# Optimization experiments

Measured on AMD Instinct MI355X. Metric: run time of the kernel, lower is better.

The kernel has to match this reference:

```python
import jax, jax.numpy as jnp
import numpy as np

DIM = 1024
NUM_HEADS = 16
HEAD_DIM = DIM // NUM_HEADS

def setup_inputs() -> dict:
    key = jax.random.key(0)
    ks = jax.random.split(key, 5)
    s = 1.0 / np.sqrt(DIM)
    x = jax.random.normal(ks[0], (2, 2048, DIM), dtype=jnp.float32)
    W_qkv = jax.random.uniform(ks[1], (DIM, 3 * DIM), dtype=jnp.float32, minval=-s, maxval=s)
    b_qkv = jax.random.uniform(ks[2], (3 * DIM,), dtype=jnp.float32, minval=-s, maxval=s)
    W_out = jax.random.uniform(ks[3], (DIM, DIM), dtype=jnp.float32, minval=-s, maxval=s)
    b_out = jax.random.uniform(ks[4], (DIM,), dtype=jnp.float32, minval=-s, maxval=s)
    return {"x": x, "W_qkv": W_qkv, "b_qkv": b_qkv, "W_out": W_out, "b_out": b_out}

def reference(x, W_qkv, b_qkv, W_out, b_out):
    B, S, _ = x.shape
    qkv = x @ W_qkv + b_qkv                       # [B,S,3*dim]
    q, k, v = jnp.split(qkv, 3, axis=-1)
    # [B,S,dim] -> [B,H,S,hd]
    def to_heads(t):
        return t.reshape(B, S, NUM_HEADS, HEAD_DIM).transpose(0, 2, 1, 3)
    q, k, v = to_heads(q), to_heads(k), to_heads(v)
    scale = HEAD_DIM ** -0.5
    scores = jnp.einsum('bhqd,bhkd->bhqk', q, k) * scale
    attn = jax.nn.softmax(scores, axis=-1)
    out = jnp.einsum('bhqk,bhkd->bhqd', attn, v)  # [B,H,S,hd]
    out = out.transpose(0, 2, 1, 3).reshape(B, S, DIM)
    return out @ W_out + b_out
```

## Files before the change

### kernel.cpp

```cpp
#include <hip/hip_runtime.h>
#include <math.h>

#define DIMM    1024
#define NHEADS  16
#define HDIM    64
#define BATCH   2
#define SEQ     2048
#define ROWS    (BATCH*SEQ)

typedef _Float16 f16x8 __attribute__((ext_vector_type(8)));
typedef _Float16 f16x4 __attribute__((ext_vector_type(4)));
typedef float    f32x4 __attribute__((ext_vector_type(4)));

__device__ inline void gl_lds16(const void* g, void* l) {
    __builtin_amdgcn_global_load_lds(
        (const __attribute__((address_space(1))) void*)g,
        (__attribute__((address_space(3))) void*)l, 16, 0, 0);
}

__global__ __launch_bounds__(256)
void cvt_kernel(const float* __restrict__ in, _Float16* __restrict__ out, int n8)
{
    int i = blockIdx.x * 256 + threadIdx.x;
    if (i >= n8) return;
    const float4 a = *(const float4*)(in + (size_t)i * 8);
    const float4 b = *(const float4*)(in + (size_t)i * 8 + 4);
    f16x8 o;
    o[0] = (_Float16)a.x; o[1] = (_Float16)a.y; o[2] = (_Float16)a.z; o[3] = (_Float16)a.w;
    o[4] = (_Float16)b.x; o[5] = (_Float16)b.y; o[6] = (_Float16)b.z; o[7] = (_Float16)b.w;
    *(f16x8*)(out + (size_t)i * 8) = o;
}

__global__ __launch_bounds__(256)
void transpose_cvt_kernel(const float* __restrict__ in, _Float16* __restrict__ out,
                          int K, int N)
{
    __shared__ float tile[64][65];
    const int k0 = blockIdx.y * 64, n0 = blockIdx.x * 64;
    const int t = threadIdx.x;
    {
        const int c4 = (t & 15) * 4;
        const int r  = t >> 4;
        #pragma unroll
        for (int i = 0; i < 4; i++) {
            const int rr = r + 16 * i;
            float4 v = *(const float4*)(in + (size_t)(k0 + rr) * N + n0 + c4);
            tile[rr][c4] = v.x; tile[rr][c4 + 1] = v.y;
            tile[rr][c4 + 2] = v.z; tile[rr][c4 + 3] = v.w;
        }
    }
    __syncthreads();
    #pragma unroll
    for (int i = 0; i < 2; i++) {
        const int seg = t + 256 * i;
        const int n   = seg >> 3;
        const int kc  = (seg & 7) * 8;
        f16x8 o;
        #pragma unroll
        for (int j = 0; j < 8; j++) o[j] = (_Float16)tile[kc + j][n];
        *(f16x8*)(out + (size_t)(n0 + n) * K + k0 + kc) = o;
    }
}

__global__ __launch_bounds__(256)
void vtranspose_kernel(const _Float16* __restrict__ qkvh, _Float16* __restrict__ vt)
{
    __shared__ _Float16 tile[64][72];
    const int kt = blockIdx.x;
    const int bh = blockIdx.y;
    const int b  = bh >> 4, h = bh & 15;
    const int t  = threadIdx.x;
    {
        const int key = t >> 2, c4 = (t & 3) * 16;
        const _Float16* src = qkvh + ((size_t)(b * SEQ + kt * 64 + key)) * (3 * DIMM)
                              + 2 * DIMM + h * HDIM + c4;
        f16x8 v0 = *(const f16x8*)src;
        f16x8 v1 = *(const f16x8*)(src + 8);
        #pragma unroll
        for (int j = 0; j < 8; j++) {
            tile[c4 + j][key]     = v0[j];
            tile[c4 + 8 + j][key] = v1[j];
        }
    }
    __syncthreads();
    {
        const int d = t >> 2, k4 = (t & 3) * 16;
        f16x8 o0, o1;
        #pragma unroll
        for (int j = 0; j < 8; j++) { o0[j] = tile[d][k4 + j]; o1[j] = tile[d][k4 + 8 + j]; }
        _Float16* dst = vt + ((size_t)bh * 64 + d) * SEQ + kt * 64 + k4;
        *(f16x8*)dst       = o0;
        *(f16x8*)(dst + 8) = o1;
    }
}

template<int OUT_F16>
__global__ __launch_bounds__(256)
void hgemm_bias_kernel(const _Float16* __restrict__ A, const _Float16* __restrict__ Bt,
                       const float* __restrict__ bias, void* __restrict__ Cout,
                       int N, int K)
{
    __shared__ _Float16 As[128 * 32];
    __shared__ _Float16 Bs[128 * 32];

    const int t    = threadIdx.x;
    const int w    = t >> 6, lane = t & 63;
    const int quad = lane >> 4, l16 = lane & 15;
    const int wr   = w >> 1, wc = w & 1;
    const int row0 = blockIdx.y * 128, col0 = blockIdx.x * 128;

    f32x4 acc[4][4];
    #pragma unroll
    for (int i = 0; i < 4; i++)
        #pragma unroll
        for (int j = 0; j < 4; j++)
            #pragma unroll
            for (int r = 0; r < 4; r++) acc[i][j][r] = 0.f;

    const int p0 = w * 128 + lane;
    const int p1 = p0 + 64;
    const int rA0 = p0 >> 2, kq0 = (p0 & 3) ^ ((p0 >> 4) & 3);
    const int rA1 = p1 >> 2, kq1 = (p1 & 3) ^ ((p1 >> 4) & 3);

    const _Float16* gA0 = A  + (size_t)(row0 + rA0) * K + kq0 * 8;
    const _Float16* gA1 = A  + (size_t)(row0 + rA1) * K + kq1 * 8;
    const _Float16* gB0 = Bt + (size_t)(col0 + rA0) * K + kq0 * 8;
    const _Float16* gB1 = Bt + (size_t)(col0 + rA1) * K + kq1 * 8;
    _Float16* lA0 = As + p0 * 8;
    _Float16* lA1 = As + p1 * 8;
    _Float16* lB0 = Bs + p0 * 8;
    _Float16* lB1 = Bs + p1 * 8;

    const int sx    = quad ^ ((l16 >> 2) & 3);
    const int abase = ((wr * 64 + l16) * 4 + sx) * 8;
    const int bbase = ((wc * 64 + l16) * 4 + sx) * 8;

    const int niter = K >> 5;
    for (int it = 0; it < niter; it++) {
        __syncthreads();
        gl_lds16(gA0, lA0); gl_lds16(gA1, lA1);
        gl_lds16(gB0, lB0); gl_lds16(gB1, lB1);
        gA0 += 32; gA1 += 32; gB0 += 32; gB1 += 32;
        __syncthreads();

        f16x8 af[4], bf[4];
        #pragma unroll
        for (int i = 0; i < 4; i++) {
            af[i] = *(const f16x8*)(As + abase + i * 512);
            bf[i] = *(const f16x8*)(Bs + bbase + i * 512);
        }
        #pragma unroll
        for (int i = 0; i < 4; i++)
            #pragma unroll
            for (int j = 0; j < 4; j++)
                acc[i][j] = __builtin_amdgcn_mfma_f32_16x16x32_f16(af[i], bf[j], acc[i][j], 0, 0, 0);
    }

    #pragma unroll
    for (int j = 0; j < 4; j++) {
        const int col = col0 + wc * 64 + j * 16 + l16;
        const float bv = bias[col];
        #pragma unroll
        for (int i = 0; i < 4; i++) {
            const int row = row0 + wr * 64 + i * 16 + quad * 4;
            #pragma unroll
            for (int r = 0; r < 4; r++) {
                const float v = acc[i][j][r] + bv;
                if (OUT_F16)
                    ((_Float16*)Cout)[(size_t)(row + r) * N + col] = (_Float16)v;
                else
                    ((float*)Cout)[(size_t)(row + r) * N + col] = v;
            }
        }
    }
}

__global__ __launch_bounds__(256, 4)
void flash_attn_kernel(const _Float16* __restrict__ qkv,
                       const _Float16* __restrict__ vtg,
                       _Float16* __restrict__ out)
{
    const int qt = blockIdx.x;
    const int bh = blockIdx.y;
    const int b  = bh >> 4, h = bh & 15;
    const int t    = threadIdx.x;
    const int w    = t >> 6;
    const int lane = t & 63;
    const int quad = lane >> 4;
    const int l16  = lane & 15;
    const int sw   = l16 & 7;

    __shared__ __align__(16) _Float16 Qs [64 * 64];
    __shared__ __align__(16) _Float16 Ks [64 * 64];
    __shared__ __align__(16) _Float16 Vts[64 * 64];
    __shared__ __align__(16) _Float16 Ps [64 * 72];

    const int q0 = qt * 64;
    const size_t rstr = 3 * DIMM;
    const _Float16* qbase = qkv + (size_t)b * SEQ * rstr;

    #pragma unroll
    for (int i = 0; i < 2; i++) {
        const int seg = t + 256 * i;
        const int row = seg >> 3, bp = seg & 7;
        const int lb  = bp ^ (row & 7);
        gl_lds16(qbase + (size_t)(q0 + row) * rstr + h * HDIM + lb * 8, Qs + seg * 8);
    }

    f32x4 Oacc[4];
    #pragma unroll
    for (int i = 0; i < 4; i++) Oacc[i] = (f32x4){0.f, 0.f, 0.f, 0.f};
    float lrow[4] = {0.f, 0.f, 0.f, 0.f};

    const int seg0 = t, seg1 = t + 256;
    const int r0 = seg0 >> 3, lb0 = (seg0 & 7) ^ (r0 & 7);
    const int r1 = seg1 >> 3, lb1 = (seg1 & 7) ^ (r1 & 7);
    const _Float16* gK0 = qbase + (size_t)r0 * rstr + DIMM + h * HDIM + lb0 * 8;
    const _Float16* gK1 = qbase + (size_t)r1 * rstr + DIMM + h * HDIM + lb1 * 8;
    const _Float16* gV0 = vtg + ((size_t)bh * 64 + r0) * SEQ + lb0 * 8;
    const _Float16* gV1 = vtg + ((size_t)bh * 64 + r1) * SEQ + lb1 * 8;

    const int kAbase = (16 * w + l16) * 64;
    const int pAbase = (16 * w + l16) * 72;

    #pragma unroll 1
    for (int k0 = 0; k0 < SEQ; k0 += 64) {
        __syncthreads();
        gl_lds16(gK0 + (size_t)k0 * rstr, Ks  + seg0 * 8);
        gl_lds16(gK1 + (size_t)k0 * rstr, Ks  + seg1 * 8);
        gl_lds16(gV0 + k0,                Vts + seg0 * 8);
        gl_lds16(gV1 + k0,                Vts + seg1 * 8);
        __syncthreads();

        f16x8 kf0 = *(const f16x8*)(Ks + kAbase + ((0 + quad) ^ sw) * 8);
        f16x8 kf1 = *(const f16x8*)(Ks + kAbase + ((4 + quad) ^ sw) * 8);
        #pragma unroll
        for (int qb = 0; qb < 4; qb++) {
            const int qrow = qb * 16 + l16;
            f16x8 qf0 = *(const f16x8*)(Qs + qrow * 64 + ((0 + quad) ^ sw) * 8);
            f16x8 qf1 = *(const f16x8*)(Qs + qrow * 64 + ((4 + quad) ^ sw) * 8);
            f32x4 s = (f32x4){0.f, 0.f, 0.f, 0.f};
            s = __builtin_amdgcn_mfma_f32_16x16x32_f16(kf0, qf0, s, 0, 0, 0);
            s = __builtin_amdgcn_mfma_f32_16x16x32_f16(kf1, qf1, s, 0, 0, 0);
            float p0 = __expf(s[0] * 0.125f);
            float p1 = __expf(s[1] * 0.125f);
            float p2 = __expf(s[2] * 0.125f);
            float p3 = __expf(s[3] * 0.125f);
            lrow[qb] += (p0 + p1) + (p2 + p3);
            f16x4 pk;
            pk[0] = (_Float16)p0; pk[1] = (_Float16)p1;
            pk[2] = (_Float16)p2; pk[3] = (_Float16)p3;
            *(f16x4*)(Ps + qrow * 72 + 16 * w + 4 * quad) = pk;
        }
        __syncthreads();

        f16x8 pf0 = *(const f16x8*)(Ps + pAbase + quad * 8);
        f16x8 pf1 = *(const f16x8*)(Ps + pAbase + 32 + quad * 8);
        #pragma unroll
        for (int db = 0; db < 4; db++) {
            const int vrow = db * 16 + l16;
            f16x8 vf0 = *(const f16x8*)(Vts + vrow * 64 + ((0 + quad) ^ sw) * 8);
            f16x8 vf1 = *(const f16x8*)(Vts + vrow * 64 + ((4 + quad) ^ sw) * 8);
            Oacc[db] = __builtin_amdgcn_mfma_f32_16x16x32_f16(pf0, vf0, Oacc[db], 0, 0, 0);
            Oacc[db] = __builtin_amdgcn_mfma_f32_16x16x32_f16(pf1, vf1, Oacc[db], 0, 0, 0);
        }
    }

    #pragma unroll
    for (int qb = 0; qb < 4; qb++) {
        lrow[qb] += __shfl_xor(lrow[qb], 16);
        lrow[qb] += __shfl_xor(lrow[qb], 32);
    }
    __syncthreads();
    float* lbuf = (float*)Ks;
    if (lane < 16) {
        #pragma unroll
        for (int qb = 0; qb < 4; qb++) lbuf[w * 64 + qb * 16 + lane] = lrow[qb];
    }
    __syncthreads();
    const int qloc = 16 * w + quad * 4;
    float lrec[4];
    #pragma unroll
    for (int r = 0; r < 4; r++) {
        const int q = qloc + r;
        lrec[r] = 1.f / (lbuf[q] + lbuf[64 + q] + lbuf[128 + q] + lbuf[192 + q]);
    }
    #pragma unroll
    for (int db = 0; db < 4; db++) {
        #pragma unroll
        for (int r = 0; r < 4; r++) {
            out[(size_t)(b * SEQ + q0 + qloc + r) * DIMM + h * HDIM + db * 16 + l16] =
                (_Float16)(Oacc[db][r] * lrec[r]);
        }
    }
}

extern "C" void kernel_launch(void* const* d_in, const int* in_sizes, int n_in,
                              void* d_out, int out_size, void* d_ws, size_t ws_size,
                              hipStream_t stream)
{
    const float* x    = (const float*)d_in[0];
    const float* Wqkv = (const float*)d_in[1];
    const float* bqkv = (const float*)d_in[2];
    const float* Wout = (const float*)d_in[3];
    const float* bout = (const float*)d_in[4];
    float* out = (float*)d_out;

    _Float16* qkvh  = (_Float16*)d_ws;
    _Float16* attnh = qkvh  + (size_t)ROWS * 3 * DIMM;
    _Float16* xh    = attnh + (size_t)ROWS * DIMM;
    _Float16* wqkvt = xh    + (size_t)ROWS * DIMM;
    _Float16* woutt = wqkvt + (size_t)3 * DIMM * DIMM;
    _Float16* vtg   = woutt + (size_t)DIMM * DIMM;

    cvt_kernel<<<(ROWS * DIMM / 8 + 255) / 256, 256, 0, stream>>>(x, xh, ROWS * DIMM / 8);
    {
        dim3 g1(3 * DIMM / 64, DIMM / 64);
        transpose_cvt_kernel<<<g1, 256, 0, stream>>>(Wqkv, wqkvt, DIMM, 3 * DIMM);
        dim3 g2(DIMM / 64, DIMM / 64);
        transpose_cvt_kernel<<<g2, 256, 0, stream>>>(Wout, woutt, DIMM, DIMM);
    }
    {
        dim3 grid(3 * DIMM / 128, ROWS / 128);
        hgemm_bias_kernel<1><<<grid, 256, 0, stream>>>(xh, wqkvt, bqkv, qkvh, 3 * DIMM, DIMM);
    }
    {
        dim3 grid(SEQ / 64, BATCH * NHEADS);
        vtranspose_kernel<<<grid, 256, 0, stream>>>(qkvh, vtg);
    }
    {
        dim3 grid(SEQ / 64, BATCH * NHEADS);
        flash_attn_kernel<<<grid, 256, 0, stream>>>(qkvh, vtg, attnh);
    }
    {
        dim3 grid(DIMM / 128, ROWS / 128);
        hgemm_bias_kernel<0><<<grid, 256, 0, stream>>>(attnh, woutt, bout, out, DIMM, DIMM);
    }
}
```

Baseline: 215.8 us.

## Fuse prep kernels, deepen GEMM K-tile to 64, keep Q fragments in registers

Merges the three conversion/transpose launches into one prep kernel that dispatches by block index, removing two launches and letting the conversion work overlap. The fp16 GEMM K-tile grows from 32 to 64 with an XOR swizzle, halving the number of barrier pairs per output tile at the cost of twice the LDS. Flash attention now loads the Q fragments straight from global memory into registers instead of staging them in LDS, which raises register pressure under the 4-blocks-per-CU launch bound.

```diff
diff --git a/kernel.cpp b/kernel.cpp
--- a/kernel.cpp
+++ b/kernel.cpp
@@ -18,26 +18,9 @@
         (__attribute__((address_space(3))) void*)l, 16, 0, 0);
 }
 
-__global__ __launch_bounds__(256)
-void cvt_kernel(const float* __restrict__ in, _Float16* __restrict__ out, int n8)
-{
-    int i = blockIdx.x * 256 + threadIdx.x;
-    if (i >= n8) return;
-    const float4 a = *(const float4*)(in + (size_t)i * 8);
-    const float4 b = *(const float4*)(in + (size_t)i * 8 + 4);
-    f16x8 o;
-    o[0] = (_Float16)a.x; o[1] = (_Float16)a.y; o[2] = (_Float16)a.z; o[3] = (_Float16)a.w;
-    o[4] = (_Float16)b.x; o[5] = (_Float16)b.y; o[6] = (_Float16)b.z; o[7] = (_Float16)b.w;
-    *(f16x8*)(out + (size_t)i * 8) = o;
-}
-
-__global__ __launch_bounds__(256)
-void transpose_cvt_kernel(const float* __restrict__ in, _Float16* __restrict__ out,
-                          int K, int N)
-{
-    __shared__ float tile[64][65];
-    const int k0 = blockIdx.y * 64, n0 = blockIdx.x * 64;
-    const int t = threadIdx.x;
+__device__ void tcvt64(const float* __restrict__ in, _Float16* __restrict__ out,
+                       int K, int N, int k0, int n0, float (*tile)[65], int t)
+{
     {
         const int c4 = (t & 15) * 4;
         const int r  = t >> 4;
@@ -63,6 +46,33 @@
 }
 
 __global__ __launch_bounds__(256)
+void prep_kernel(const float* __restrict__ x, const float* __restrict__ Wqkv,
+                 const float* __restrict__ Wout, _Float16* __restrict__ xh,
+                 _Float16* __restrict__ wqkvt, _Float16* __restrict__ woutt)
+{
+    __shared__ float tile[64][65];
+    const int bx = blockIdx.x;
+    const int t  = threadIdx.x;
+    if (bx < 2048) {
+        const int i = bx * 256 + t;
+        const float4 a = *(const float4*)(x + (size_t)i * 8);
+        const float4 b = *(const float4*)(x + (size_t)i * 8 + 4);
+        f16x8 o;
+        o[0] = (_Float16)a.x; o[1] = (_Float16)a.y; o[2] = (_Float16)a.z; o[3] = (_Float16)a.w;
+        o[4] = (_Float16)b.x; o[5] = (_Float16)b.y; o[6] = (_Float16)b.z; o[7] = (_Float16)b.w;
+        *(f16x8*)(xh + (size_t)i * 8) = o;
+    } else if (bx < 2816) {
+        const int id = bx - 2048;
+        const int gx = id % 48, gy = id / 48;
+        tcvt64(Wqkv, wqkvt, DIMM, 3 * DIMM, gy * 64, gx * 64, tile, t);
+    } else {
+        const int id = bx - 2816;
+        const int gx = id & 15, gy = id >> 4;
+        tcvt64(Wout, woutt, DIMM, DIMM, gy * 64, gx * 64, tile, t);
+    }
+}
+
+__global__ __launch_bounds__(256)
 void vtranspose_kernel(const _Float16* __restrict__ qkvh, _Float16* __restrict__ vt)
 {
     __shared__ _Float16 tile[64][72];
@@ -100,14 +110,15 @@
                        const float* __restrict__ bias, void* __restrict__ Cout,
                        int N, int K)
 {
-    __shared__ _Float16 As[128 * 32];
-    __shared__ _Float16 Bs[128 * 32];
+    __shared__ _Float16 As[128 * 64];
+    __shared__ _Float16 Bs[128 * 64];
 
     const int t    = threadIdx.x;
     const int w    = t >> 6, lane = t & 63;
     const int quad = lane >> 4, l16 = lane & 15;
     const int wr   = w >> 1, wc = w & 1;
     const int row0 = blockIdx.y * 128, col0 = blockIdx.x * 128;
+    const int sw   = l16 & 7;
 
     f32x4 acc[4][4];
     #pragma unroll
@@ -117,43 +128,49 @@
             #pragma unroll
             for (int r = 0; r < 4; r++) acc[i][j][r] = 0.f;
 
-    const int p0 = w * 128 + lane;
-    const int p1 = p0 + 64;
-    const int rA0 = p0 >> 2, kq0 = (p0 & 3) ^ ((p0 >> 4) & 3);
-    const int rA1 = p1 >> 2, kq1 = (p1 & 3) ^ ((p1 >> 4) & 3);
-
-    const _Float16* gA0 = A  + (size_t)(row0 + rA0) * K + kq0 * 8;
-    const _Float16* gA1 = A  + (size_t)(row0 + rA1) * K + kq1 * 8;
-    const _Float16* gB0 = Bt + (size_t)(col0 + rA0) * K + kq0 * 8;
-    const _Float16* gB1 = Bt + (size_t)(col0 + rA1) * K + kq1 * 8;
-    _Float16* lA0 = As + p0 * 8;
-    _Float16* lA1 = As + p1 * 8;
-    _Float16* lB0 = Bs + p0 * 8;
-    _Float16* lB1 = Bs + p1 * 8;
-
-    const int sx    = quad ^ ((l16 >> 2) & 3);
-    const int abase = ((wr * 64 + l16) * 4 + sx) * 8;
-    const int bbase = ((wc * 64 + l16) * 4 + sx) * 8;
-
-    const int niter = K >> 5;
+    const _Float16* gA[4];
+    const _Float16* gB[4];
+    int lofs[4];
+    #pragma unroll
+    for (int j = 0; j < 4; j++) {
+        const int s   = t + 256 * j;
+        const int row = s >> 3;
+        const int kb  = (s & 7) ^ (row & 7);
+        gA[j] = A  + (size_t)(row0 + row) * K + kb * 8;
+        gB[j] = Bt + (size_t)(col0 + row) * K + kb * 8;
+        lofs[j] = s * 8;
+    }
+
+    const int niter = K >> 6;
+    #pragma unroll 1
     for (int it = 0; it < niter; it++) {
         __syncthreads();
-        gl_lds16(gA0, lA0); gl_lds16(gA1, lA1);
-        gl_lds16(gB0, lB0); gl_lds16(gB1, lB1);
-        gA0 += 32; gA1 += 32; gB0 += 32; gB1 += 32;
-        __syncthreads();
-
-        f16x8 af[4], bf[4];
+        #pragma unroll
+        for (int j = 0; j < 4; j++) gl_lds16(gA[j], As + lofs[j]);
+        #pragma unroll
+        for (int j = 0; j < 4; j++) gl_lds16(gB[j], Bs + lofs[j]);
+        #pragma unroll
+        for (int j = 0; j < 4; j++) { gA[j] += 64; gB[j] += 64; }
+        __syncthreads();
+
+        f16x8 af[4][2], bf[4][2];
         #pragma unroll
         for (int i = 0; i < 4; i++) {
-            af[i] = *(const f16x8*)(As + abase + i * 512);
-            bf[i] = *(const f16x8*)(Bs + bbase + i * 512);
+            const int arow = wr * 64 + i * 16 + l16;
+            const int brow = wc * 64 + i * 16 + l16;
+            #pragma unroll
+            for (int hh = 0; hh < 2; hh++) {
+                af[i][hh] = *(const f16x8*)(As + (arow * 8 + ((hh * 4 + quad) ^ sw)) * 8);
+                bf[i][hh] = *(const f16x8*)(Bs + (brow * 8 + ((hh * 4 + quad) ^ sw)) * 8);
+            }
         }
         #pragma unroll
         for (int i = 0; i < 4; i++)
             #pragma unroll
-            for (int j = 0; j < 4; j++)
-                acc[i][j] = __builtin_amdgcn_mfma_f32_16x16x32_f16(af[i], bf[j], acc[i][j], 0, 0, 0);
+            for (int j = 0; j < 4; j++) {
+                acc[i][j] = __builtin_amdgcn_mfma_f32_16x16x32_f16(af[i][0], bf[j][0], acc[i][j], 0, 0, 0);
+                acc[i][j] = __builtin_amdgcn_mfma_f32_16x16x32_f16(af[i][1], bf[j][1], acc[i][j], 0, 0, 0);
+            }
     }
 
     #pragma unroll
@@ -190,7 +207,6 @@
     const int l16  = lane & 15;
     const int sw   = l16 & 7;
 
-    __shared__ __align__(16) _Float16 Qs [64 * 64];
     __shared__ __align__(16) _Float16 Ks [64 * 64];
     __shared__ __align__(16) _Float16 Vts[64 * 64];
     __shared__ __align__(16) _Float16 Ps [64 * 72];
@@ -199,12 +215,12 @@
     const size_t rstr = 3 * DIMM;
     const _Float16* qbase = qkv + (size_t)b * SEQ * rstr;
 
-    #pragma unroll
-    for (int i = 0; i < 2; i++) {
-        const int seg = t + 256 * i;
-        const int row = seg >> 3, bp = seg & 7;
-        const int lb  = bp ^ (row & 7);
-        gl_lds16(qbase + (size_t)(q0 + row) * rstr + h * HDIM + lb * 8, Qs + seg * 8);
+    f16x8 qf[4][2];
+    #pragma unroll
+    for (int qb = 0; qb < 4; qb++) {
+        const _Float16* qrow = qbase + (size_t)(q0 + qb * 16 + l16) * rstr + h * HDIM;
+        qf[qb][0] = *(const f16x8*)(qrow + quad * 8);
+        qf[qb][1] = *(const f16x8*)(qrow + 32 + quad * 8);
     }
 
     f32x4 Oacc[4];
@@ -236,12 +252,9 @@
         f16x8 kf1 = *(const f16x8*)(Ks + kAbase + ((4 + quad) ^ sw) * 8);
         #pragma unroll
         for (int qb = 0; qb < 4; qb++) {
-            const int qrow = qb * 16 + l16;
-            f16x8 qf0 = *(const f16x8*)(Qs + qrow * 64 + ((0 + quad) ^ sw) * 8);
-            f16x8 qf1 = *(const f16x8*)(Qs + qrow * 64 + ((4 + quad) ^ sw) * 8);
             f32x4 s = (f32x4){0.f, 0.f, 0.f, 0.f};
-            s = __builtin_amdgcn_mfma_f32_16x16x32_f16(kf0, qf0, s, 0, 0, 0);
-            s = __builtin_amdgcn_mfma_f32_16x16x32_f16(kf1, qf1, s, 0, 0, 0);
+            s = __builtin_amdgcn_mfma_f32_16x16x32_f16(kf0, qf[qb][0], s, 0, 0, 0);
+            s = __builtin_amdgcn_mfma_f32_16x16x32_f16(kf1, qf[qb][1], s, 0, 0, 0);
             float p0 = __expf(s[0] * 0.125f);
             float p1 = __expf(s[1] * 0.125f);
             float p2 = __expf(s[2] * 0.125f);
@@ -250,7 +263,7 @@
             f16x4 pk;
             pk[0] = (_Float16)p0; pk[1] = (_Float16)p1;
             pk[2] = (_Float16)p2; pk[3] = (_Float16)p3;
-            *(f16x4*)(Ps + qrow * 72 + 16 * w + 4 * quad) = pk;
+            *(f16x4*)(Ps + (qb * 16 + l16) * 72 + 16 * w + 4 * quad) = pk;
         }
         __syncthreads();
 
@@ -313,13 +326,7 @@
     _Float16* woutt = wqkvt + (size_t)3 * DIMM * DIMM;
     _Float16* vtg   = woutt + (size_t)DIMM * DIMM;
 
-    cvt_kernel<<<(ROWS * DIMM / 8 + 255) / 256, 256, 0, stream>>>(x, xh, ROWS * DIMM / 8);
-    {
-        dim3 g1(3 * DIMM / 64, DIMM / 64);
-        transpose_cvt_kernel<<<g1, 256, 0, stream>>>(Wqkv, wqkvt, DIMM, 3 * DIMM);
-        dim3 g2(DIMM / 64, DIMM / 64);
-        transpose_cvt_kernel<<<g2, 256, 0, stream>>>(Wout, woutt, DIMM, DIMM);
-    }
+    prep_kernel<<<3072, 256, 0, stream>>>(x, Wqkv, Wout, xh, wqkvt, woutt);
     {
         dim3 grid(3 * DIMM / 128, ROWS / 128);
         hgemm_bias_kernel<1><<<grid, 256, 0, stream>>>(xh, wqkvt, bqkv, qkvh, 3 * DIMM, DIMM);
```

After: 206.3 us. 1.05x faster.

## Fuse prep kernels, write V transposed from QKV GEMM, keep Q in registers

Applied to the files above, without the earlier changes.

Merges the x conversion and both weight transpose-converts into one prep kernel, which cuts two launches. The QKV GEMM epilogue now writes V blocks directly in the transposed per-head layout, so the separate V transpose kernel goes away. Flash attention loads Q fragments straight into registers instead of staging them in LDS, which frees LDS and removes per-iteration LDS reads. It also uses exp2f with the log2e factor folded into the scale. The trade-offs are more register pressure, and V is stored as 4-element strided writes from the GEMM epilogue.

```diff
diff --git a/kernel.cpp b/kernel.cpp
--- a/kernel.cpp
+++ b/kernel.cpp
@@ -18,26 +18,9 @@
         (__attribute__((address_space(3))) void*)l, 16, 0, 0);
 }
 
-__global__ __launch_bounds__(256)
-void cvt_kernel(const float* __restrict__ in, _Float16* __restrict__ out, int n8)
-{
-    int i = blockIdx.x * 256 + threadIdx.x;
-    if (i >= n8) return;
-    const float4 a = *(const float4*)(in + (size_t)i * 8);
-    const float4 b = *(const float4*)(in + (size_t)i * 8 + 4);
-    f16x8 o;
-    o[0] = (_Float16)a.x; o[1] = (_Float16)a.y; o[2] = (_Float16)a.z; o[3] = (_Float16)a.w;
-    o[4] = (_Float16)b.x; o[5] = (_Float16)b.y; o[6] = (_Float16)b.z; o[7] = (_Float16)b.w;
-    *(f16x8*)(out + (size_t)i * 8) = o;
-}
-
-__global__ __launch_bounds__(256)
-void transpose_cvt_kernel(const float* __restrict__ in, _Float16* __restrict__ out,
-                          int K, int N)
-{
-    __shared__ float tile[64][65];
-    const int k0 = blockIdx.y * 64, n0 = blockIdx.x * 64;
-    const int t = threadIdx.x;
+__device__ void tcvt64(const float* __restrict__ in, _Float16* __restrict__ out,
+                       int K, int N, int k0, int n0, float (*tile)[65], int t)
+{
     {
         const int c4 = (t & 15) * 4;
         const int r  = t >> 4;
@@ -63,42 +46,37 @@
 }
 
 __global__ __launch_bounds__(256)
-void vtranspose_kernel(const _Float16* __restrict__ qkvh, _Float16* __restrict__ vt)
-{
-    __shared__ _Float16 tile[64][72];
-    const int kt = blockIdx.x;
-    const int bh = blockIdx.y;
-    const int b  = bh >> 4, h = bh & 15;
+void prep_kernel(const float* __restrict__ x, const float* __restrict__ Wqkv,
+                 const float* __restrict__ Wout, _Float16* __restrict__ xh,
+                 _Float16* __restrict__ wqkvt, _Float16* __restrict__ woutt)
+{
+    __shared__ float tile[64][65];
+    const int bx = blockIdx.x;
     const int t  = threadIdx.x;
-    {
-        const int key = t >> 2, c4 = (t & 3) * 16;
-        const _Float16* src = qkvh + ((size_t)(b * SEQ + kt * 64 + key)) * (3 * DIMM)
-                              + 2 * DIMM + h * HDIM + c4;
-        f16x8 v0 = *(const f16x8*)src;
-        f16x8 v1 = *(const f16x8*)(src + 8);
-        #pragma unroll
-        for (int j = 0; j < 8; j++) {
-            tile[c4 + j][key]     = v0[j];
-            tile[c4 + 8 + j][key] = v1[j];
-        }
-    }
-    __syncthreads();
-    {
-        const int d = t >> 2, k4 = (t & 3) * 16;
-        f16x8 o0, o1;
-        #pragma unroll
-        for (int j = 0; j < 8; j++) { o0[j] = tile[d][k4 + j]; o1[j] = tile[d][k4 + 8 + j]; }
-        _Float16* dst = vt + ((size_t)bh * 64 + d) * SEQ + kt * 64 + k4;
-        *(f16x8*)dst       = o0;
-        *(f16x8*)(dst + 8) = o1;
-    }
-}
-
-template<int OUT_F16>
+    if (bx < 2048) {
+        const int i = bx * 256 + t;
+        const float4 a = *(const float4*)(x + (size_t)i * 8);
+        const float4 b = *(const float4*)(x + (size_t)i * 8 + 4);
+        f16x8 o;
+        o[0] = (_Float16)a.x; o[1] = (_Float16)a.y; o[2] = (_Float16)a.z; o[3] = (_Float16)a.w;
+        o[4] = (_Float16)b.x; o[5] = (_Float16)b.y; o[6] = (_Float16)b.z; o[7] = (_Float16)b.w;
+        *(f16x8*)(xh + (size_t)i * 8) = o;
+    } else if (bx < 2816) {
+        const int id = bx - 2048;
+        const int gx = id % 48, gy = id / 48;
+        tcvt64(Wqkv, wqkvt, DIMM, 3 * DIMM, gy * 64, gx * 64, tile, t);
+    } else {
+        const int id = bx - 2816;
+        const int gx = id & 15, gy = id >> 4;
+        tcvt64(Wout, woutt, DIMM, DIMM, gy * 64, gx * 64, tile, t);
+    }
+}
+
+template<int MODE>
 __global__ __launch_bounds__(256)
 void hgemm_bias_kernel(const _Float16* __restrict__ A, const _Float16* __restrict__ Bt,
                        const float* __restrict__ bias, void* __restrict__ Cout,
-                       int N, int K)
+                       _Float16* __restrict__ vtg, int N, int K)
 {
     __shared__ _Float16 As[128 * 32];
     __shared__ _Float16 Bs[128 * 32];
@@ -156,6 +134,7 @@
                 acc[i][j] = __builtin_amdgcn_mfma_f32_16x16x32_f16(af[i], bf[j], acc[i][j], 0, 0, 0);
     }
 
+    const bool vblock = (MODE == 1) && (col0 >= 2 * DIMM);
     #pragma unroll
     for (int j = 0; j < 4; j++) {
         const int col = col0 + wc * 64 + j * 16 + l16;
@@ -163,13 +142,23 @@
         #pragma unroll
         for (int i = 0; i < 4; i++) {
             const int row = row0 + wr * 64 + i * 16 + quad * 4;
-            #pragma unroll
-            for (int r = 0; r < 4; r++) {
-                const float v = acc[i][j][r] + bv;
-                if (OUT_F16)
-                    ((_Float16*)Cout)[(size_t)(row + r) * N + col] = (_Float16)v;
-                else
-                    ((float*)Cout)[(size_t)(row + r) * N + col] = v;
+            if (vblock) {
+                const int dg  = col - 2 * DIMM;
+                const int h   = dg >> 6, dl = dg & 63;
+                const int b   = row >> 11, key = row & (SEQ - 1);
+                f16x4 o;
+                #pragma unroll
+                for (int r = 0; r < 4; r++) o[r] = (_Float16)(acc[i][j][r] + bv);
+                *(f16x4*)(vtg + ((size_t)((b * NHEADS + h) * 64 + dl)) * SEQ + key) = o;
+            } else {
+                #pragma unroll
+                for (int r = 0; r < 4; r++) {
+                    const float v = acc[i][j][r] + bv;
+                    if (MODE == 1)
+                        ((_Float16*)Cout)[(size_t)(row + r) * N + col] = (_Float16)v;
+                    else
+                        ((float*)Cout)[(size_t)(row + r) * N + col] = v;
+                }
             }
         }
     }
@@ -190,7 +179,6 @@
     const int l16  = lane & 15;
     const int sw   = l16 & 7;
 
-    __shared__ __align__(16) _Float16 Qs [64 * 64];
     __shared__ __align__(16) _Float16 Ks [64 * 64];
     __shared__ __align__(16) _Float16 Vts[64 * 64];
     __shared__ __align__(16) _Float16 Ps [64 * 72];
@@ -199,12 +187,12 @@
     const size_t rstr = 3 * DIMM;
     const _Float16* qbase = qkv + (size_t)b * SEQ * rstr;
 
-    #pragma unroll
-    for (int i = 0; i < 2; i++) {
-        const int seg = t + 256 * i;
-        const int row = seg >> 3, bp = seg & 7;
-        const int lb  = bp ^ (row & 7);
-        gl_lds16(qbase + (size_t)(q0 + row) * rstr + h * HDIM + lb * 8, Qs + seg * 8);
+    f16x8 qf[4][2];
+    #pragma unroll
+    for (int qb = 0; qb < 4; qb++) {
+        const _Float16* qrow = qbase + (size_t)(q0 + qb * 16 + l16) * rstr + h * HDIM;
+        qf[qb][0] = *(const f16x8*)(qrow + quad * 8);
+        qf[qb][1] = *(const f16x8*)(qrow + 32 + quad * 8);
     }
 
     f32x4 Oacc[4];
@@ -222,6 +210,7 @@
 
     const int kAbase = (16 * w + l16) * 64;
     const int pAbase = (16 * w + l16) * 72;
+    const float SCL  = 0.18033688f;
 
     #pragma unroll 1
     for (int k0 = 0; k0 < SEQ; k0 += 64) {
@@ -236,21 +225,18 @@
         f16x8 kf1 = *(const f16x8*)(Ks + kAbase + ((4 + quad) ^ sw) * 8);
         #pragma unroll
         for (int qb = 0; qb < 4; qb++) {
-            const int qrow = qb * 16 + l16;
-            f16x8 qf0 = *(const f16x8*)(Qs + qrow * 64 + ((0 + quad) ^ sw) * 8);
-            f16x8 qf1 = *(const f16x8*)(Qs + qrow * 64 + ((4 + quad) ^ sw) * 8);
             f32x4 s = (f32x4){0.f, 0.f, 0.f, 0.f};
-            s = __builtin_amdgcn_mfma_f32_16x16x32_f16(kf0, qf0, s, 0, 0, 0);
-            s = __builtin_amdgcn_mfma_f32_16x16x32_f16(kf1, qf1, s, 0, 0, 0);
-            float p0 = __expf(s[0] * 0.125f);
-            float p1 = __expf(s[1] * 0.125f);
-            float p2 = __expf(s[2] * 0.125f);
-            float p3 = __expf(s[3] * 0.125f);
+            s = __builtin_amdgcn_mfma_f32_16x16x32_f16(kf0, qf[qb][0], s, 0, 0, 0);
+            s = __builtin_amdgcn_mfma_f32_16x16x32_f16(kf1, qf[qb][1], s, 0, 0, 0);
+            float p0 = exp2f(s[0] * SCL);
+            float p1 = exp2f(s[1] * SCL);
+            float p2 = exp2f(s[2] * SCL);
+            float p3 = exp2f(s[3] * SCL);
             lrow[qb] += (p0 + p1) + (p2 + p3);
             f16x4 pk;
             pk[0] = (_Float16)p0; pk[1] = (_Float16)p1;
             pk[2] = (_Float16)p2; pk[3] = (_Float16)p3;
-            *(f16x4*)(Ps + qrow * 72 + 16 * w + 4 * quad) = pk;
+            *(f16x4*)(Ps + (qb * 16 + l16) * 72 + 16 * w + 4 * quad) = pk;
         }
         __syncthreads();
 
@@ -313,20 +299,10 @@
     _Float16* woutt = wqkvt + (size_t)3 * DIMM * DIMM;
     _Float16* vtg   = woutt + (size_t)DIMM * DIMM;
 
-    cvt_kernel<<<(ROWS * DIMM / 8 + 255) / 256, 256, 0, stream>>>(x, xh, ROWS * DIMM / 8);
-    {
-        dim3 g1(3 * DIMM / 64, DIMM / 64);
-        transpose_cvt_kernel<<<g1, 256, 0, stream>>>(Wqkv, wqkvt, DIMM, 3 * DIMM);
-        dim3 g2(DIMM / 64, DIMM / 64);
-        transpose_cvt_kernel<<<g2, 256, 0, stream>>>(Wout, woutt, DIMM, DIMM);
-    }
+    prep_kernel<<<3072, 256, 0, stream>>>(x, Wqkv, Wout, xh, wqkvt, woutt);
     {
         dim3 grid(3 * DIMM / 128, ROWS / 128);
-        hgemm_bias_kernel<1><<<grid, 256, 0, stream>>>(xh, wqkvt, bqkv, qkvh, 3 * DIMM, DIMM);
-    }
-    {
-        dim3 grid(SEQ / 64, BATCH * NHEADS);
-        vtranspose_kernel<<<grid, 256, 0, stream>>>(qkvh, vtg);
+        hgemm_bias_kernel<1><<<grid, 256, 0, stream>>>(xh, wqkvt, bqkv, qkvh, vtg, 3 * DIMM, DIMM);
     }
     {
         dim3 grid(SEQ / 64, BATCH * NHEADS);
@@ -334,6 +310,6 @@
     }
     {
         dim3 grid(DIMM / 128, ROWS / 128);
-        hgemm_bias_kernel<0><<<grid, 256, 0, stream>>>(attnh, woutt, bout, out, DIMM, DIMM);
-    }
-}
+        hgemm_bias_kernel<0><<<grid, 256, 0, stream>>>(attnh, woutt, bout, out, nullptr, DIMM, DIMM);
+    }
+}
```

Result: no change. 214.5 us (-0.6%).
